# Kernel tuning notes

Measured on AMD Instinct MI355X. Metric: run time of the kernel, lower is better.

Reference implementation:

```python
import jax, jax.numpy as jnp
import numpy as np

N = 4096      # n_nodes
F = 512       # input_dim
R = 64        # repr_dim
H = 8         # n_heads
EPS_BIAS = 0.01
ALPHA = 0.2   # LeakyReLU negative slope
NEG_BIG = 1e16


def setup_inputs() -> dict:
    key = jax.random.key(0)
    k1, k2, k3, k4, k5 = jax.random.split(key, 5)
    node_matrix = jax.random.normal(k1, (N, F), dtype=jnp.float32)
    adjacency_matrix = (jax.random.uniform(k2, (N, N)) < 0.01).astype(jnp.float32)
    adjacency_matrix = jnp.maximum(adjacency_matrix, jnp.eye(N, dtype=jnp.float32))
    # learned parameters (xavier-ish scale)
    W = jax.random.normal(k3, (H, F, R), dtype=jnp.float32) * 0.06
    shared_attention = jax.random.normal(k4, (H, 2 * R), dtype=jnp.float32) * 0.1
    attention_biases = jax.random.normal(k5, (N, N), dtype=jnp.float32) * 0.02
    return {
        "node_matrix": node_matrix,
        "adjacency_matrix": adjacency_matrix,
        "W": W,
        "shared_attention": shared_attention,
        "attention_biases": attention_biases,
    }


def reference(node_matrix, adjacency_matrix, W, shared_attention, attention_biases):
    # hidden_repr: [H, N, R]
    hidden = jnp.einsum('nf,hfr->hnr', node_matrix, W)
    # per-head source/destination scores: [H, N]
    a_src = jnp.einsum('hnr,hr->hn', hidden, shared_attention[:, :R])
    a_dst = jnp.einsum('hnr,hr->hn', hidden, shared_attention[:, R:])
    # broadcast-sum + trainable pair bias: [H, N, N]
    pre = a_src[:, :, None] + a_dst[:, None, :] + EPS_BIAS * attention_biases[None]
    full = jnp.where(pre >= 0, pre, ALPHA * pre)  # LeakyReLU
    # adjacency masking then row softmax
    scores = full + (-NEG_BIG * (1.0 - adjacency_matrix))[None]
    att = jax.nn.softmax(scores, axis=-1)  # [H, N, N]
    # weighted aggregation: [H, N, R]
    out = jnp.einsum('hnm,hmr->hnr', att, hidden)
    # 'concat' aggregation: [N, H*R], head h occupies columns h*R:(h+1)*R
    return jnp.transpose(out, (1, 0, 2)).reshape(N, H * R)
```

## Files before the change

kernel.cpp:

```cpp
#include <hip/hip_runtime.h>
#include <hip/hip_bf16.h>

#define NN 4096
#define FF 512
#define RR 64
#define HH 8
#define HR (HH * RR)
#define CAP 128
#define ATT_STRIDE 144

typedef short bf16x8 __attribute__((ext_vector_type(8)));
typedef float f32x4 __attribute__((ext_vector_type(4)));

__device__ __forceinline__ unsigned short f2bf(float f) {
  __hip_bfloat16 h = __float2bfloat16(f);
  return *reinterpret_cast<unsigned short*>(&h);
}
__device__ __forceinline__ float bf2f(unsigned short u) {
  union { unsigned u32; float f; } cv;
  cv.u32 = ((unsigned)u) << 16;
  return cv.f;
}
__device__ __forceinline__ unsigned nib4(const float4 v) {
  unsigned m = 0;
  if (v.x != 0.f) m |= 1u;
  if (v.y != 0.f) m |= 2u;
  if (v.z != 0.f) m |= 4u;
  if (v.w != 0.f) m |= 8u;
  return m;
}

__global__ __launch_bounds__(256) void k_stream(
    const float* __restrict__ X, const float* __restrict__ W,
    const float* __restrict__ adj,
    unsigned short* __restrict__ Xb, unsigned short* __restrict__ BbT,
    int* __restrict__ colsG, int* __restrict__ cnts)
{
  __shared__ unsigned short wt[64][68];
  const int b = blockIdx.x;
  const int tid = threadIdx.x;

  if (b < 1024) {
    const int lane = tid & 63;
    const int row = b * 4 + (tid >> 6);
    const float* arow = adj + (size_t)row * NN;
    unsigned long long pm = 0;
    {
      float4 buf[8];
#pragma unroll
      for (int c = 0; c < 8; ++c)
        buf[c] = *reinterpret_cast<const float4*>(&arow[c * 256 + (lane << 2)]);
#pragma unroll
      for (int c = 0; c < 8; ++c)
        pm |= (unsigned long long)nib4(buf[c]) << (4 * c);
#pragma unroll
      for (int c = 0; c < 8; ++c)
        buf[c] = *reinterpret_cast<const float4*>(&arow[(c + 8) * 256 + (lane << 2)]);
#pragma unroll
      for (int c = 0; c < 8; ++c)
        pm |= (unsigned long long)nib4(buf[c]) << (4 * c + 32);
    }
    const int cnt = __popcll(pm);
    int pfx = cnt;
#pragma unroll
    for (int off = 1; off < 64; off <<= 1) {
      const int o = __shfl_up(pfx, off);
      if (lane >= off) pfx += o;
    }
    int pos = pfx - cnt;
    unsigned long long m = pm;
    int* cg = colsG + (size_t)row * CAP;
    while (m) {
      const int bit = (int)__builtin_ctzll(m);
      m &= m - 1;
      if (pos < CAP) cg[pos] = ((bit >> 2) << 8) + (lane << 2) + (bit & 3);
      ++pos;
    }
    const int tot = __shfl(pfx, 63);
    for (int p = tot + lane; p < CAP; p += 64) cg[p] = 0;
    if (lane == 63) cnts[row] = tot < CAP ? tot : CAP;
  } else if (b < 3072) {
    const int t = (b - 1024) * 256 + tid;
    const float4 v = reinterpret_cast<const float4*>(X)[t];
    ushort4 u;
    u.x = f2bf(v.x); u.y = f2bf(v.y); u.z = f2bf(v.z); u.w = f2bf(v.w);
    reinterpret_cast<ushort4*>(Xb)[t] = u;
  } else {
    const int b2 = b - 3072;
    const int h = b2 >> 3;
    const int f0 = (b2 & 7) << 6;
    const int fr = tid >> 2;
    const int rq = (tid & 3) << 4;
    const float* wp = W + (size_t)h * FF * RR + (size_t)(f0 + fr) * RR + rq;
#pragma unroll
    for (int v = 0; v < 4; ++v) {
      const float4 x = *reinterpret_cast<const float4*>(wp + v * 4);
      wt[rq + v * 4 + 0][fr] = f2bf(x.x);
      wt[rq + v * 4 + 1][fr] = f2bf(x.y);
      wt[rq + v * 4 + 2][fr] = f2bf(x.z);
      wt[rq + v * 4 + 3][fr] = f2bf(x.w);
    }
    __syncthreads();
    const int r = tid >> 2;
    unsigned short* op = BbT + (size_t)(h * 64 + r) * FF + f0 + ((tid & 3) << 4);
    int4 w0 = *reinterpret_cast<const int4*>(&wt[r][(tid & 3) << 4]);
    int4 w1 = *reinterpret_cast<const int4*>(&wt[r][((tid & 3) << 4) + 8]);
    *reinterpret_cast<int4*>(op) = w0;
    *reinterpret_cast<int4*>(op + 8) = w1;
  }
}

__global__ __launch_bounds__(256) void k_gemm_hidden(
    const unsigned short* __restrict__ Xb,
    const unsigned short* __restrict__ BbT,
    const float* __restrict__ sa,
    unsigned short* __restrict__ hiddenT,
    float* __restrict__ a_srcT,
    float* __restrict__ a_dstT)
{
  const int row0 = blockIdx.x * 64;
  const int h = blockIdx.y;
  const int n0 = h * 64;
  __shared__ unsigned short Als[64 * 32];
  __shared__ unsigned short Bls[64 * 32];
  __shared__ float redS[64][2];
  __shared__ float redD[64][2];
  const int tid = threadIdx.x;
  const int l = tid & 63;
  const int wid = tid >> 6;
  const int wr = wid >> 1, wc = wid & 1;

  f32x4 acc[2][2];
#pragma unroll
  for (int a = 0; a < 2; ++a)
#pragma unroll
    for (int bb = 0; bb < 2; ++bb) acc[a][bb] = (f32x4){0.f, 0.f, 0.f, 0.f};

  const int srow = tid >> 2;
  const int skel = (tid & 3) * 8;

  for (int k0 = 0; k0 < FF; k0 += 32) {
    const int4 av = *reinterpret_cast<const int4*>(
        &Xb[(size_t)(row0 + srow) * FF + k0 + skel]);
    const int4 bv = *reinterpret_cast<const int4*>(
        &BbT[(size_t)(n0 + srow) * FF + k0 + skel]);
    __syncthreads();
    *reinterpret_cast<int4*>(&Als[tid * 8]) = av;
    *reinterpret_cast<int4*>(&Bls[tid * 8]) = bv;
    __syncthreads();

    const int ka = (l >> 4) * 8;
    const bf16x8 a0 = *reinterpret_cast<const bf16x8*>(&Als[(32 * wr + 0  + (l & 15)) * 32 + ka]);
    const bf16x8 a1 = *reinterpret_cast<const bf16x8*>(&Als[(32 * wr + 16 + (l & 15)) * 32 + ka]);
    const bf16x8 b0 = *reinterpret_cast<const bf16x8*>(&Bls[(32 * wc + 0  + (l & 15)) * 32 + ka]);
    const bf16x8 b1 = *reinterpret_cast<const bf16x8*>(&Bls[(32 * wc + 16 + (l & 15)) * 32 + ka]);
    acc[0][0] = __builtin_amdgcn_mfma_f32_16x16x32_bf16(a0, b0, acc[0][0], 0, 0, 0);
    acc[0][1] = __builtin_amdgcn_mfma_f32_16x16x32_bf16(a0, b1, acc[0][1], 0, 0, 0);
    acc[1][0] = __builtin_amdgcn_mfma_f32_16x16x32_bf16(a1, b0, acc[1][0], 0, 0, 0);
    acc[1][1] = __builtin_amdgcn_mfma_f32_16x16x32_bf16(a1, b1, acc[1][1], 0, 0, 0);
  }

  const int lg = l >> 4;
  const int lc = l & 15;

#pragma unroll
  for (int mi = 0; mi < 2; ++mi)
#pragma unroll
    for (int ni = 0; ni < 2; ++ni)
#pragma unroll
      for (int j = 0; j < 4; ++j) {
        const int rowg = row0 + 32 * wr + 16 * mi + (lg << 2) + j;
        const int colg = n0 + 32 * wc + 16 * ni + lc;
        hiddenT[(size_t)rowg * HR + colg] = f2bf(acc[mi][ni][j]);
      }

  float sS[2], sD[2];
#pragma unroll
  for (int ni = 0; ni < 2; ++ni) {
    const int col = 32 * wc + 16 * ni + lc;
    sS[ni] = sa[(size_t)h * 2 * RR + col];
    sD[ni] = sa[(size_t)h * 2 * RR + RR + col];
  }
#pragma unroll
  for (int mi = 0; mi < 2; ++mi)
#pragma unroll
    for (int j = 0; j < 4; ++j) {
      float ps = acc[mi][0][j] * sS[0] + acc[mi][1][j] * sS[1];
      float pd = acc[mi][0][j] * sD[0] + acc[mi][1][j] * sD[1];
#pragma unroll
      for (int off = 8; off >= 1; off >>= 1) {
        ps += __shfl_xor(ps, off);
        pd += __shfl_xor(pd, off);
      }
      if (lc == 0) {
        const int rl = 32 * wr + 16 * mi + (lg << 2) + j;
        redS[rl][wc] = ps;
        redD[rl][wc] = pd;
      }
    }
  __syncthreads();
  if (tid < 64) {
    a_srcT[(size_t)(row0 + tid) * HH + h] = redS[tid][0] + redS[tid][1];
    a_dstT[(size_t)(row0 + tid) * HH + h] = redD[tid][0] + redD[tid][1];
  }
}

__global__ __launch_bounds__(256) void k_gat_row(
    const int* __restrict__ colsG,
    const int* __restrict__ cnts,
    const float* __restrict__ bias,
    const float* __restrict__ a_srcT,
    const float* __restrict__ a_dstT,
    const unsigned short* __restrict__ hiddenT,
    float* __restrict__ out)
{
  const int i = blockIdx.x;
  const int tid = threadIdx.x;

  __shared__ __align__(16) float att[HH][ATT_STRIDE];
  __shared__ int cols[CAP];
  __shared__ __align__(16) float accred[4][HR];

  int c = 0;
  float4 d0, d1;
  float b = 0.f;
  if (tid < CAP) {
    c = colsG[(size_t)i * CAP + tid];
  }
  const int count = cnts[i];
  if (tid < CAP) {
    b = 0.01f * bias[(size_t)i * NN + c];
    d0 = *reinterpret_cast<const float4*>(&a_dstT[(size_t)c * HH]);
    d1 = *reinterpret_cast<const float4*>(&a_dstT[(size_t)c * HH + 4]);
  }
  const float4 s0 = *reinterpret_cast<const float4*>(&a_srcT[(size_t)i * HH]);
  const float4 s1 = *reinterpret_cast<const float4*>(&a_srcT[(size_t)i * HH + 4]);

  if (tid < CAP) {
    cols[tid] = c;
    float s;
    s = s0.x + d0.x + b; att[0][tid] = (s >= 0.f) ? s : 0.2f * s;
    s = s0.y + d0.y + b; att[1][tid] = (s >= 0.f) ? s : 0.2f * s;
    s = s0.z + d0.z + b; att[2][tid] = (s >= 0.f) ? s : 0.2f * s;
    s = s0.w + d0.w + b; att[3][tid] = (s >= 0.f) ? s : 0.2f * s;
    s = s1.x + d1.x + b; att[4][tid] = (s >= 0.f) ? s : 0.2f * s;
    s = s1.y + d1.y + b; att[5][tid] = (s >= 0.f) ? s : 0.2f * s;
    s = s1.z + d1.z + b; att[6][tid] = (s >= 0.f) ? s : 0.2f * s;
    s = s1.w + d1.w + b; att[7][tid] = (s >= 0.f) ? s : 0.2f * s;
  }
  __syncthreads();

  {
    const int g = tid >> 5;
    const int l = tid & 31;
    float* arow_h = att[g];
    float m = -3.0e38f;
    for (int t = l; t < count; t += 32) m = fmaxf(m, arow_h[t]);
#pragma unroll
    for (int o = 16; o >= 1; o >>= 1) m = fmaxf(m, __shfl_xor(m, o));
    float ssum = 0.f;
    for (int t = l; t < count; t += 32) {
      const float e = expf(arow_h[t] - m);
      arow_h[t] = e;
      ssum += e;
    }
#pragma unroll
    for (int o = 16; o >= 1; o >>= 1) ssum += __shfl_xor(ssum, o);
    const float inv = 1.0f / ssum;
    for (int t = l; t < count; t += 32) arow_h[t] *= inv;
  }
  __syncthreads();

  {
    const int g2 = tid >> 6;
    const int o0 = (tid & 63) << 3;
    const float* attrow = att[o0 >> 6];
    const unsigned short* hb = hiddenT + o0;
    const int q = (count + 3) >> 2;
    const int t0 = g2 * q;
    const int t1 = min(t0 + q, count);
    float4 accA = make_float4(0.f, 0.f, 0.f, 0.f);
    float4 accB = make_float4(0.f, 0.f, 0.f, 0.f);
    for (int t = t0; t < t1; ++t) {
      const int cc = cols[t];
      const float a = attrow[t];
      const ushort4 ua = *reinterpret_cast<const ushort4*>(hb + (size_t)cc * HR);
      const ushort4 ub = *reinterpret_cast<const ushort4*>(hb + (size_t)cc * HR + 4);
      accA.x += a * bf2f(ua.x); accA.y += a * bf2f(ua.y);
      accA.z += a * bf2f(ua.z); accA.w += a * bf2f(ua.w);
      accB.x += a * bf2f(ub.x); accB.y += a * bf2f(ub.y);
      accB.z += a * bf2f(ub.z); accB.w += a * bf2f(ub.w);
    }
    *reinterpret_cast<float4*>(&accred[g2][o0]) = accA;
    *reinterpret_cast<float4*>(&accred[g2][o0 + 4]) = accB;
  }
  __syncthreads();
  {
    const int o = tid << 1;
    const float2 r = make_float2(
        accred[0][o] + accred[1][o] + accred[2][o] + accred[3][o],
        accred[0][o + 1] + accred[1][o + 1] + accred[2][o + 1] + accred[3][o + 1]);
    *reinterpret_cast<float2*>(&out[(size_t)i * HR + o]) = r;
  }
}

extern "C" void kernel_launch(void* const* d_in, const int* in_sizes, int n_in,
                              void* d_out, int out_size, void* d_ws, size_t ws_size,
                              hipStream_t stream) {
  const float* X    = (const float*)d_in[0];
  const float* adj  = (const float*)d_in[1];
  const float* W    = (const float*)d_in[2];
  const float* sa   = (const float*)d_in[3];
  const float* bias = (const float*)d_in[4];
  float* out = (float*)d_out;

  unsigned short* hiddenT = (unsigned short*)d_ws;
  unsigned short* Xb  = hiddenT + (size_t)NN * HR;
  unsigned short* BbT = Xb + (size_t)NN * FF;
  float* a_srcT = (float*)(BbT + (size_t)HR * FF);
  float* a_dstT = a_srcT + (size_t)NN * HH;
  int* cnts     = (int*)(a_dstT + (size_t)NN * HH);
  int* colsG    = cnts + NN;

  k_stream<<<dim3(3136), 256, 0, stream>>>(X, W, adj, Xb, BbT, colsG, cnts);
  k_gemm_hidden<<<dim3(NN / 64, HH), 256, 0, stream>>>(Xb, BbT, sa, hiddenT, a_srcT, a_dstT);
  k_gat_row<<<dim3(NN), 256, 0, stream>>>(colsG, cnts, bias, a_srcT, a_dstT, hiddenT, out);
}
```

Baseline: 47.00 us.

## Fuse X bf16 conversion into GEMM and co-schedule with adjacency compaction

Drops the separate pass that writes a bf16 copy of X. The GEMM now reads fp32 X and converts it inline, and it runs in the same launch as the adjacency compaction blocks, with the W transpose split into a small kernel of its own. This removes one round trip of X through memory and lets the GEMM overlap the adjacency streaming. Separately, the aggregation in the row kernel is split 8 ways with 16 columns per thread instead of 4 ways, which raises register use and the size of the reduction in shared memory.

```diff
diff --git a/kernel.cpp b/kernel.cpp
--- a/kernel.cpp
+++ b/kernel.cpp
@@ -30,19 +30,137 @@
   return m;
 }
 
-__global__ __launch_bounds__(256) void k_stream(
-    const float* __restrict__ X, const float* __restrict__ W,
-    const float* __restrict__ adj,
-    unsigned short* __restrict__ Xb, unsigned short* __restrict__ BbT,
+__global__ __launch_bounds__(256) void k_wconv(
+    const float* __restrict__ W, unsigned short* __restrict__ BbT)
+{
+  __shared__ unsigned short wt[64][68];
+  const int b2 = blockIdx.x;
+  const int h = b2 >> 3;
+  const int f0 = (b2 & 7) << 6;
+  const int tid = threadIdx.x;
+  const int fr = tid >> 2;
+  const int rq = (tid & 3) << 4;
+  const float* wp = W + (size_t)h * FF * RR + (size_t)(f0 + fr) * RR + rq;
+#pragma unroll
+  for (int v = 0; v < 4; ++v) {
+    const float4 x = *reinterpret_cast<const float4*>(wp + v * 4);
+    wt[rq + v * 4 + 0][fr] = f2bf(x.x);
+    wt[rq + v * 4 + 1][fr] = f2bf(x.y);
+    wt[rq + v * 4 + 2][fr] = f2bf(x.z);
+    wt[rq + v * 4 + 3][fr] = f2bf(x.w);
+  }
+  __syncthreads();
+  const int r = tid >> 2;
+  unsigned short* op = BbT + (size_t)(h * 64 + r) * FF + f0 + ((tid & 3) << 4);
+  int4 w0 = *reinterpret_cast<const int4*>(&wt[r][(tid & 3) << 4]);
+  int4 w1 = *reinterpret_cast<const int4*>(&wt[r][((tid & 3) << 4) + 8]);
+  *reinterpret_cast<int4*>(op) = w0;
+  *reinterpret_cast<int4*>(op + 8) = w1;
+}
+
+__global__ __launch_bounds__(256) void k_mega(
+    const float* __restrict__ X, const float* __restrict__ adj,
+    const float* __restrict__ sa, const unsigned short* __restrict__ BbT,
+    unsigned short* __restrict__ hiddenT,
+    float* __restrict__ a_srcT, float* __restrict__ a_dstT,
     int* __restrict__ colsG, int* __restrict__ cnts)
 {
-  __shared__ unsigned short wt[64][68];
+  __shared__ unsigned short Als[64 * 32];
+  __shared__ unsigned short Bls[64 * 32];
+  __shared__ float redS[64][2];
+  __shared__ float redD[64][2];
   const int b = blockIdx.x;
   const int tid = threadIdx.x;
 
-  if (b < 1024) {
+  if (b < 512) {
+    const int row0 = (b & 63) * 64;
+    const int h = b >> 6;
+    const int n0 = h * 64;
+    const int l = tid & 63;
+    const int wid = tid >> 6;
+    const int wr = wid >> 1, wc = wid & 1;
+
+    f32x4 acc[2][2];
+#pragma unroll
+    for (int a = 0; a < 2; ++a)
+#pragma unroll
+      for (int bb = 0; bb < 2; ++bb) acc[a][bb] = (f32x4){0.f, 0.f, 0.f, 0.f};
+
+    const int srow = tid >> 2;
+    const int skel = (tid & 3) * 8;
+
+    for (int k0 = 0; k0 < FF; k0 += 32) {
+      const float* xp = &X[(size_t)(row0 + srow) * FF + k0 + skel];
+      const float4 x0 = *reinterpret_cast<const float4*>(xp);
+      const float4 x1 = *reinterpret_cast<const float4*>(xp + 4);
+      const int4 bv = *reinterpret_cast<const int4*>(
+          &BbT[(size_t)(n0 + srow) * FF + k0 + skel]);
+      ushort4 ua, ub;
+      ua.x = f2bf(x0.x); ua.y = f2bf(x0.y); ua.z = f2bf(x0.z); ua.w = f2bf(x0.w);
+      ub.x = f2bf(x1.x); ub.y = f2bf(x1.y); ub.z = f2bf(x1.z); ub.w = f2bf(x1.w);
+      __syncthreads();
+      *reinterpret_cast<ushort4*>(&Als[tid * 8]) = ua;
+      *reinterpret_cast<ushort4*>(&Als[tid * 8 + 4]) = ub;
+      *reinterpret_cast<int4*>(&Bls[tid * 8]) = bv;
+      __syncthreads();
+
+      const int ka = (l >> 4) * 8;
+      const bf16x8 a0 = *reinterpret_cast<const bf16x8*>(&Als[(32 * wr + 0  + (l & 15)) * 32 + ka]);
+      const bf16x8 a1 = *reinterpret_cast<const bf16x8*>(&Als[(32 * wr + 16 + (l & 15)) * 32 + ka]);
+      const bf16x8 b0 = *reinterpret_cast<const bf16x8*>(&Bls[(32 * wc + 0  + (l & 15)) * 32 + ka]);
+      const bf16x8 b1 = *reinterpret_cast<const bf16x8*>(&Bls[(32 * wc + 16 + (l & 15)) * 32 + ka]);
+      acc[0][0] = __builtin_amdgcn_mfma_f32_16x16x32_bf16(a0, b0, acc[0][0], 0, 0, 0);
+      acc[0][1] = __builtin_amdgcn_mfma_f32_16x16x32_bf16(a0, b1, acc[0][1], 0, 0, 0);
+      acc[1][0] = __builtin_amdgcn_mfma_f32_16x16x32_bf16(a1, b0, acc[1][0], 0, 0, 0);
+      acc[1][1] = __builtin_amdgcn_mfma_f32_16x16x32_bf16(a1, b1, acc[1][1], 0, 0, 0);
+    }
+
+    const int lg = l >> 4;
+    const int lc = l & 15;
+
+#pragma unroll
+    for (int mi = 0; mi < 2; ++mi)
+#pragma unroll
+      for (int ni = 0; ni < 2; ++ni)
+#pragma unroll
+        for (int j = 0; j < 4; ++j) {
+          const int rowg = row0 + 32 * wr + 16 * mi + (lg << 2) + j;
+          const int colg = n0 + 32 * wc + 16 * ni + lc;
+          hiddenT[(size_t)rowg * HR + colg] = f2bf(acc[mi][ni][j]);
+        }
+
+    float sS[2], sD[2];
+#pragma unroll
+    for (int ni = 0; ni < 2; ++ni) {
+      const int col = 32 * wc + 16 * ni + lc;
+      sS[ni] = sa[(size_t)h * 2 * RR + col];
+      sD[ni] = sa[(size_t)h * 2 * RR + RR + col];
+    }
+#pragma unroll
+    for (int mi = 0; mi < 2; ++mi)
+#pragma unroll
+      for (int j = 0; j < 4; ++j) {
+        float ps = acc[mi][0][j] * sS[0] + acc[mi][1][j] * sS[1];
+        float pd = acc[mi][0][j] * sD[0] + acc[mi][1][j] * sD[1];
+#pragma unroll
+        for (int off = 8; off >= 1; off >>= 1) {
+          ps += __shfl_xor(ps, off);
+          pd += __shfl_xor(pd, off);
+        }
+        if (lc == 0) {
+          const int rl = 32 * wr + 16 * mi + (lg << 2) + j;
+          redS[rl][wc] = ps;
+          redD[rl][wc] = pd;
+        }
+      }
+    __syncthreads();
+    if (tid < 64) {
+      a_srcT[(size_t)(row0 + tid) * HH + h] = redS[tid][0] + redS[tid][1];
+      a_dstT[(size_t)(row0 + tid) * HH + h] = redD[tid][0] + redD[tid][1];
+    }
+  } else {
     const int lane = tid & 63;
-    const int row = b * 4 + (tid >> 6);
+    const int row = (b - 512) * 4 + (tid >> 6);
     const float* arow = adj + (size_t)row * NN;
     unsigned long long pm = 0;
     {
@@ -79,129 +197,6 @@
     const int tot = __shfl(pfx, 63);
     for (int p = tot + lane; p < CAP; p += 64) cg[p] = 0;
     if (lane == 63) cnts[row] = tot < CAP ? tot : CAP;
-  } else if (b < 3072) {
-    const int t = (b - 1024) * 256 + tid;
-    const float4 v = reinterpret_cast<const float4*>(X)[t];
-    ushort4 u;
-    u.x = f2bf(v.x); u.y = f2bf(v.y); u.z = f2bf(v.z); u.w = f2bf(v.w);
-    reinterpret_cast<ushort4*>(Xb)[t] = u;
-  } else {
-    const int b2 = b - 3072;
-    const int h = b2 >> 3;
-    const int f0 = (b2 & 7) << 6;
-    const int fr = tid >> 2;
-    const int rq = (tid & 3) << 4;
-    const float* wp = W + (size_t)h * FF * RR + (size_t)(f0 + fr) * RR + rq;
-#pragma unroll
-    for (int v = 0; v < 4; ++v) {
-      const float4 x = *reinterpret_cast<const float4*>(wp + v * 4);
-      wt[rq + v * 4 + 0][fr] = f2bf(x.x);
-      wt[rq + v * 4 + 1][fr] = f2bf(x.y);
-      wt[rq + v * 4 + 2][fr] = f2bf(x.z);
-      wt[rq + v * 4 + 3][fr] = f2bf(x.w);
-    }
-    __syncthreads();
-    const int r = tid >> 2;
-    unsigned short* op = BbT + (size_t)(h * 64 + r) * FF + f0 + ((tid & 3) << 4);
-    int4 w0 = *reinterpret_cast<const int4*>(&wt[r][(tid & 3) << 4]);
-    int4 w1 = *reinterpret_cast<const int4*>(&wt[r][((tid & 3) << 4) + 8]);
-    *reinterpret_cast<int4*>(op) = w0;
-    *reinterpret_cast<int4*>(op + 8) = w1;
-  }
-}
-
-__global__ __launch_bounds__(256) void k_gemm_hidden(
-    const unsigned short* __restrict__ Xb,
-    const unsigned short* __restrict__ BbT,
-    const float* __restrict__ sa,
-    unsigned short* __restrict__ hiddenT,
-    float* __restrict__ a_srcT,
-    float* __restrict__ a_dstT)
-{
-  const int row0 = blockIdx.x * 64;
-  const int h = blockIdx.y;
-  const int n0 = h * 64;
-  __shared__ unsigned short Als[64 * 32];
-  __shared__ unsigned short Bls[64 * 32];
-  __shared__ float redS[64][2];
-  __shared__ float redD[64][2];
-  const int tid = threadIdx.x;
-  const int l = tid & 63;
-  const int wid = tid >> 6;
-  const int wr = wid >> 1, wc = wid & 1;
-
-  f32x4 acc[2][2];
-#pragma unroll
-  for (int a = 0; a < 2; ++a)
-#pragma unroll
-    for (int bb = 0; bb < 2; ++bb) acc[a][bb] = (f32x4){0.f, 0.f, 0.f, 0.f};
-
-  const int srow = tid >> 2;
-  const int skel = (tid & 3) * 8;
-
-  for (int k0 = 0; k0 < FF; k0 += 32) {
-    const int4 av = *reinterpret_cast<const int4*>(
-        &Xb[(size_t)(row0 + srow) * FF + k0 + skel]);
-    const int4 bv = *reinterpret_cast<const int4*>(
-        &BbT[(size_t)(n0 + srow) * FF + k0 + skel]);
-    __syncthreads();
-    *reinterpret_cast<int4*>(&Als[tid * 8]) = av;
-    *reinterpret_cast<int4*>(&Bls[tid * 8]) = bv;
-    __syncthreads();
-
-    const int ka = (l >> 4) * 8;
-    const bf16x8 a0 = *reinterpret_cast<const bf16x8*>(&Als[(32 * wr + 0  + (l & 15)) * 32 + ka]);
-    const bf16x8 a1 = *reinterpret_cast<const bf16x8*>(&Als[(32 * wr + 16 + (l & 15)) * 32 + ka]);
-    const bf16x8 b0 = *reinterpret_cast<const bf16x8*>(&Bls[(32 * wc + 0  + (l & 15)) * 32 + ka]);
-    const bf16x8 b1 = *reinterpret_cast<const bf16x8*>(&Bls[(32 * wc + 16 + (l & 15)) * 32 + ka]);
-    acc[0][0] = __builtin_amdgcn_mfma_f32_16x16x32_bf16(a0, b0, acc[0][0], 0, 0, 0);
-    acc[0][1] = __builtin_amdgcn_mfma_f32_16x16x32_bf16(a0, b1, acc[0][1], 0, 0, 0);
-    acc[1][0] = __builtin_amdgcn_mfma_f32_16x16x32_bf16(a1, b0, acc[1][0], 0, 0, 0);
-    acc[1][1] = __builtin_amdgcn_mfma_f32_16x16x32_bf16(a1, b1, acc[1][1], 0, 0, 0);
-  }
-
-  const int lg = l >> 4;
-  const int lc = l & 15;
-
-#pragma unroll
-  for (int mi = 0; mi < 2; ++mi)
-#pragma unroll
-    for (int ni = 0; ni < 2; ++ni)
-#pragma unroll
-      for (int j = 0; j < 4; ++j) {
-        const int rowg = row0 + 32 * wr + 16 * mi + (lg << 2) + j;
-        const int colg = n0 + 32 * wc + 16 * ni + lc;
-        hiddenT[(size_t)rowg * HR + colg] = f2bf(acc[mi][ni][j]);
-      }
-
-  float sS[2], sD[2];
-#pragma unroll
-  for (int ni = 0; ni < 2; ++ni) {
-    const int col = 32 * wc + 16 * ni + lc;
-    sS[ni] = sa[(size_t)h * 2 * RR + col];
-    sD[ni] = sa[(size_t)h * 2 * RR + RR + col];
-  }
-#pragma unroll
-  for (int mi = 0; mi < 2; ++mi)
-#pragma unroll
-    for (int j = 0; j < 4; ++j) {
-      float ps = acc[mi][0][j] * sS[0] + acc[mi][1][j] * sS[1];
-      float pd = acc[mi][0][j] * sD[0] + acc[mi][1][j] * sD[1];
-#pragma unroll
-      for (int off = 8; off >= 1; off >>= 1) {
-        ps += __shfl_xor(ps, off);
-        pd += __shfl_xor(pd, off);
-      }
-      if (lc == 0) {
-        const int rl = 32 * wr + 16 * mi + (lg << 2) + j;
-        redS[rl][wc] = ps;
-        redD[rl][wc] = pd;
-      }
-    }
-  __syncthreads();
-  if (tid < 64) {
-    a_srcT[(size_t)(row0 + tid) * HH + h] = redS[tid][0] + redS[tid][1];
-    a_dstT[(size_t)(row0 + tid) * HH + h] = redD[tid][0] + redD[tid][1];
   }
 }
 
@@ -219,14 +214,12 @@
 
   __shared__ __align__(16) float att[HH][ATT_STRIDE];
   __shared__ int cols[CAP];
-  __shared__ __align__(16) float accred[4][HR];
+  __shared__ __align__(16) float accred[8][HR];
 
   int c = 0;
   float4 d0, d1;
   float b = 0.f;
-  if (tid < CAP) {
-    c = colsG[(size_t)i * CAP + tid];
-  }
+  if (tid < CAP) c = colsG[(size_t)i * CAP + tid];
   const int count = cnts[i];
   if (tid < CAP) {
     b = 0.01f * bias[(size_t)i * NN + c];
@@ -272,35 +265,49 @@
   __syncthreads();
 
   {
-    const int g2 = tid >> 6;
-    const int o0 = (tid & 63) << 3;
+    const int g2 = tid >> 5;
+    const int o0 = (tid & 31) << 4;
     const float* attrow = att[o0 >> 6];
     const unsigned short* hb = hiddenT + o0;
-    const int q = (count + 3) >> 2;
+    const int q = (count + 7) >> 3;
     const int t0 = g2 * q;
     const int t1 = min(t0 + q, count);
-    float4 accA = make_float4(0.f, 0.f, 0.f, 0.f);
-    float4 accB = make_float4(0.f, 0.f, 0.f, 0.f);
+    float acc[16];
+#pragma unroll
+    for (int j = 0; j < 16; ++j) acc[j] = 0.f;
     for (int t = t0; t < t1; ++t) {
       const int cc = cols[t];
       const float a = attrow[t];
-      const ushort4 ua = *reinterpret_cast<const ushort4*>(hb + (size_t)cc * HR);
-      const ushort4 ub = *reinterpret_cast<const ushort4*>(hb + (size_t)cc * HR + 4);
-      accA.x += a * bf2f(ua.x); accA.y += a * bf2f(ua.y);
-      accA.z += a * bf2f(ua.z); accA.w += a * bf2f(ua.w);
-      accB.x += a * bf2f(ub.x); accB.y += a * bf2f(ub.y);
-      accB.z += a * bf2f(ub.z); accB.w += a * bf2f(ub.w);
-    }
-    *reinterpret_cast<float4*>(&accred[g2][o0]) = accA;
-    *reinterpret_cast<float4*>(&accred[g2][o0 + 4]) = accB;
+      const unsigned short* hp = hb + (size_t)cc * HR;
+      const ushort4 u0 = *reinterpret_cast<const ushort4*>(hp);
+      const ushort4 u1 = *reinterpret_cast<const ushort4*>(hp + 4);
+      const ushort4 u2 = *reinterpret_cast<const ushort4*>(hp + 8);
+      const ushort4 u3 = *reinterpret_cast<const ushort4*>(hp + 12);
+      acc[0] += a * bf2f(u0.x);  acc[1] += a * bf2f(u0.y);
+      acc[2] += a * bf2f(u0.z);  acc[3] += a * bf2f(u0.w);
+      acc[4] += a * bf2f(u1.x);  acc[5] += a * bf2f(u1.y);
+      acc[6] += a * bf2f(u1.z);  acc[7] += a * bf2f(u1.w);
+      acc[8] += a * bf2f(u2.x);  acc[9] += a * bf2f(u2.y);
+      acc[10] += a * bf2f(u2.z); acc[11] += a * bf2f(u2.w);
+      acc[12] += a * bf2f(u3.x); acc[13] += a * bf2f(u3.y);
+      acc[14] += a * bf2f(u3.z); acc[15] += a * bf2f(u3.w);
+    }
+#pragma unroll
+    for (int j = 0; j < 4; ++j) {
+      float4 v = make_float4(acc[j * 4], acc[j * 4 + 1], acc[j * 4 + 2], acc[j * 4 + 3]);
+      *reinterpret_cast<float4*>(&accred[g2][o0 + j * 4]) = v;
+    }
   }
   __syncthreads();
   {
     const int o = tid << 1;
-    const float2 r = make_float2(
-        accred[0][o] + accred[1][o] + accred[2][o] + accred[3][o],
-        accred[0][o + 1] + accred[1][o + 1] + accred[2][o + 1] + accred[3][o + 1]);
-    *reinterpret_cast<float2*>(&out[(size_t)i * HR + o]) = r;
+    float r0 = 0.f, r1 = 0.f;
+#pragma unroll
+    for (int g = 0; g < 8; ++g) {
+      const float2 v = *reinterpret_cast<const float2*>(&accred[g][o]);
+      r0 += v.x; r1 += v.y;
+    }
+    *reinterpret_cast<float2*>(&out[(size_t)i * HR + o]) = make_float2(r0, r1);
   }
 }
 
@@ -315,14 +322,13 @@
   float* out = (float*)d_out;
 
   unsigned short* hiddenT = (unsigned short*)d_ws;
-  unsigned short* Xb  = hiddenT + (size_t)NN * HR;
-  unsigned short* BbT = Xb + (size_t)NN * FF;
+  unsigned short* BbT = hiddenT + (size_t)NN * HR;
   float* a_srcT = (float*)(BbT + (size_t)HR * FF);
   float* a_dstT = a_srcT + (size_t)NN * HH;
   int* cnts     = (int*)(a_dstT + (size_t)NN * HH);
   int* colsG    = cnts + NN;
 
-  k_stream<<<dim3(3136), 256, 0, stream>>>(X, W, adj, Xb, BbT, colsG, cnts);
-  k_gemm_hidden<<<dim3(NN / 64, HH), 256, 0, stream>>>(Xb, BbT, sa, hiddenT, a_srcT, a_dstT);
+  k_wconv<<<dim3(64), 256, 0, stream>>>(W, BbT);
+  k_mega<<<dim3(1536), 256, 0, stream>>>(X, adj, sa, BbT, hiddenT, a_srcT, a_dstT, colsG, cnts);
   k_gat_row<<<dim3(NN), 256, 0, stream>>>(colsG, cnts, bias, a_srcT, a_dstT, hiddenT, out);
 }
```

Measured after the change: 48.35 us. 1.03x slower.

## Overlap adjacency compaction with hidden GEMM by merging them into one kernel

Applied to the files above, without the earlier changes.

The adjacency scan that builds the per-row column lists moves out of the convert kernel and into the GEMM kernel as extra blocks. The first 512 blocks do the GEMM and the remaining 1024 blocks compact the adjacency rows. The memory-bound 64 MB adjacency read can then run concurrently with the compute-bound GEMM, and the convert kernel becomes small. The trade-off is that the merged kernel carries the GEMM's shared-memory footprint for the scan blocks, and scheduling order depends on block dispatch.

```diff
diff --git a/kernel.cpp b/kernel.cpp
--- a/kernel.cpp
+++ b/kernel.cpp
@@ -30,19 +30,147 @@
   return m;
 }
 
-__global__ __launch_bounds__(256) void k_stream(
+__global__ __launch_bounds__(256) void k_convert(
     const float* __restrict__ X, const float* __restrict__ W,
-    const float* __restrict__ adj,
-    unsigned short* __restrict__ Xb, unsigned short* __restrict__ BbT,
-    int* __restrict__ colsG, int* __restrict__ cnts)
+    unsigned short* __restrict__ Xb, unsigned short* __restrict__ BbT)
 {
   __shared__ unsigned short wt[64][68];
   const int b = blockIdx.x;
   const int tid = threadIdx.x;
 
-  if (b < 1024) {
+  if (b < 2048) {
+    const int t = b * 256 + tid;
+    const float4 v = reinterpret_cast<const float4*>(X)[t];
+    ushort4 u;
+    u.x = f2bf(v.x); u.y = f2bf(v.y); u.z = f2bf(v.z); u.w = f2bf(v.w);
+    reinterpret_cast<ushort4*>(Xb)[t] = u;
+  } else {
+    const int b2 = b - 2048;
+    const int h = b2 >> 3;
+    const int f0 = (b2 & 7) << 6;
+    const int fr = tid >> 2;
+    const int rq = (tid & 3) << 4;
+    const float* wp = W + (size_t)h * FF * RR + (size_t)(f0 + fr) * RR + rq;
+#pragma unroll
+    for (int v = 0; v < 4; ++v) {
+      const float4 x = *reinterpret_cast<const float4*>(wp + v * 4);
+      wt[rq + v * 4 + 0][fr] = f2bf(x.x);
+      wt[rq + v * 4 + 1][fr] = f2bf(x.y);
+      wt[rq + v * 4 + 2][fr] = f2bf(x.z);
+      wt[rq + v * 4 + 3][fr] = f2bf(x.w);
+    }
+    __syncthreads();
+    const int r = tid >> 2;
+    unsigned short* op = BbT + (size_t)(h * 64 + r) * FF + f0 + ((tid & 3) << 4);
+    int4 w0 = *reinterpret_cast<const int4*>(&wt[r][(tid & 3) << 4]);
+    int4 w1 = *reinterpret_cast<const int4*>(&wt[r][((tid & 3) << 4) + 8]);
+    *reinterpret_cast<int4*>(op) = w0;
+    *reinterpret_cast<int4*>(op + 8) = w1;
+  }
+}
+
+__global__ __launch_bounds__(256) void k_mega(
+    const unsigned short* __restrict__ Xb,
+    const unsigned short* __restrict__ BbT,
+    const float* __restrict__ sa,
+    const float* __restrict__ adj,
+    unsigned short* __restrict__ hiddenT,
+    float* __restrict__ a_srcT,
+    float* __restrict__ a_dstT,
+    int* __restrict__ colsG,
+    int* __restrict__ cnts)
+{
+  __shared__ unsigned short Als[64 * 32];
+  __shared__ unsigned short Bls[64 * 32];
+  __shared__ float redS[64][2];
+  __shared__ float redD[64][2];
+  const int b = blockIdx.x;
+  const int tid = threadIdx.x;
+
+  if (b < 512) {
+    const int row0 = (b & 63) * 64;
+    const int h = b >> 6;
+    const int n0 = h * 64;
+    const int l = tid & 63;
+    const int wid = tid >> 6;
+    const int wr = wid >> 1, wc = wid & 1;
+
+    f32x4 acc[2][2];
+#pragma unroll
+    for (int a = 0; a < 2; ++a)
+#pragma unroll
+      for (int bb = 0; bb < 2; ++bb) acc[a][bb] = (f32x4){0.f, 0.f, 0.f, 0.f};
+
+    const int srow = tid >> 2;
+    const int skel = (tid & 3) * 8;
+
+    for (int k0 = 0; k0 < FF; k0 += 32) {
+      const int4 av = *reinterpret_cast<const int4*>(
+          &Xb[(size_t)(row0 + srow) * FF + k0 + skel]);
+      const int4 bv = *reinterpret_cast<const int4*>(
+          &BbT[(size_t)(n0 + srow) * FF + k0 + skel]);
+      __syncthreads();
+      *reinterpret_cast<int4*>(&Als[tid * 8]) = av;
+      *reinterpret_cast<int4*>(&Bls[tid * 8]) = bv;
+      __syncthreads();
+
+      const int ka = (l >> 4) * 8;
+      const bf16x8 a0 = *reinterpret_cast<const bf16x8*>(&Als[(32 * wr + 0  + (l & 15)) * 32 + ka]);
+      const bf16x8 a1 = *reinterpret_cast<const bf16x8*>(&Als[(32 * wr + 16 + (l & 15)) * 32 + ka]);
+      const bf16x8 b0 = *reinterpret_cast<const bf16x8*>(&Bls[(32 * wc + 0  + (l & 15)) * 32 + ka]);
+      const bf16x8 b1 = *reinterpret_cast<const bf16x8*>(&Bls[(32 * wc + 16 + (l & 15)) * 32 + ka]);
+      acc[0][0] = __builtin_amdgcn_mfma_f32_16x16x32_bf16(a0, b0, acc[0][0], 0, 0, 0);
+      acc[0][1] = __builtin_amdgcn_mfma_f32_16x16x32_bf16(a0, b1, acc[0][1], 0, 0, 0);
+      acc[1][0] = __builtin_amdgcn_mfma_f32_16x16x32_bf16(a1, b0, acc[1][0], 0, 0, 0);
+      acc[1][1] = __builtin_amdgcn_mfma_f32_16x16x32_bf16(a1, b1, acc[1][1], 0, 0, 0);
+    }
+
+    const int lg = l >> 4;
+    const int lc = l & 15;
+
+#pragma unroll
+    for (int mi = 0; mi < 2; ++mi)
+#pragma unroll
+      for (int ni = 0; ni < 2; ++ni)
+#pragma unroll
+        for (int j = 0; j < 4; ++j) {
+          const int rowg = row0 + 32 * wr + 16 * mi + (lg << 2) + j;
+          const int colg = n0 + 32 * wc + 16 * ni + lc;
+          hiddenT[(size_t)rowg * HR + colg] = f2bf(acc[mi][ni][j]);
+        }
+
+    float sS[2], sD[2];
+#pragma unroll
+    for (int ni = 0; ni < 2; ++ni) {
+      const int col = 32 * wc + 16 * ni + lc;
+      sS[ni] = sa[(size_t)h * 2 * RR + col];
+      sD[ni] = sa[(size_t)h * 2 * RR + RR + col];
+    }
+#pragma unroll
+    for (int mi = 0; mi < 2; ++mi)
+#pragma unroll
+      for (int j = 0; j < 4; ++j) {
+        float ps = acc[mi][0][j] * sS[0] + acc[mi][1][j] * sS[1];
+        float pd = acc[mi][0][j] * sD[0] + acc[mi][1][j] * sD[1];
+#pragma unroll
+        for (int off = 8; off >= 1; off >>= 1) {
+          ps += __shfl_xor(ps, off);
+          pd += __shfl_xor(pd, off);
+        }
+        if (lc == 0) {
+          const int rl = 32 * wr + 16 * mi + (lg << 2) + j;
+          redS[rl][wc] = ps;
+          redD[rl][wc] = pd;
+        }
+      }
+    __syncthreads();
+    if (tid < 64) {
+      a_srcT[(size_t)(row0 + tid) * HH + h] = redS[tid][0] + redS[tid][1];
+      a_dstT[(size_t)(row0 + tid) * HH + h] = redD[tid][0] + redD[tid][1];
+    }
+  } else {
     const int lane = tid & 63;
-    const int row = b * 4 + (tid >> 6);
+    const int row = (b - 512) * 4 + (tid >> 6);
     const float* arow = adj + (size_t)row * NN;
     unsigned long long pm = 0;
     {
@@ -79,129 +207,6 @@
     const int tot = __shfl(pfx, 63);
     for (int p = tot + lane; p < CAP; p += 64) cg[p] = 0;
     if (lane == 63) cnts[row] = tot < CAP ? tot : CAP;
-  } else if (b < 3072) {
-    const int t = (b - 1024) * 256 + tid;
-    const float4 v = reinterpret_cast<const float4*>(X)[t];
-    ushort4 u;
-    u.x = f2bf(v.x); u.y = f2bf(v.y); u.z = f2bf(v.z); u.w = f2bf(v.w);
-    reinterpret_cast<ushort4*>(Xb)[t] = u;
-  } else {
-    const int b2 = b - 3072;
-    const int h = b2 >> 3;
-    const int f0 = (b2 & 7) << 6;
-    const int fr = tid >> 2;
-    const int rq = (tid & 3) << 4;
-    const float* wp = W + (size_t)h * FF * RR + (size_t)(f0 + fr) * RR + rq;
-#pragma unroll
-    for (int v = 0; v < 4; ++v) {
-      const float4 x = *reinterpret_cast<const float4*>(wp + v * 4);
-      wt[rq + v * 4 + 0][fr] = f2bf(x.x);
-      wt[rq + v * 4 + 1][fr] = f2bf(x.y);
-      wt[rq + v * 4 + 2][fr] = f2bf(x.z);
-      wt[rq + v * 4 + 3][fr] = f2bf(x.w);
-    }
-    __syncthreads();
-    const int r = tid >> 2;
-    unsigned short* op = BbT + (size_t)(h * 64 + r) * FF + f0 + ((tid & 3) << 4);
-    int4 w0 = *reinterpret_cast<const int4*>(&wt[r][(tid & 3) << 4]);
-    int4 w1 = *reinterpret_cast<const int4*>(&wt[r][((tid & 3) << 4) + 8]);
-    *reinterpret_cast<int4*>(op) = w0;
-    *reinterpret_cast<int4*>(op + 8) = w1;
-  }
-}
-
-__global__ __launch_bounds__(256) void k_gemm_hidden(
-    const unsigned short* __restrict__ Xb,
-    const unsigned short* __restrict__ BbT,
-    const float* __restrict__ sa,
-    unsigned short* __restrict__ hiddenT,
-    float* __restrict__ a_srcT,
-    float* __restrict__ a_dstT)
-{
-  const int row0 = blockIdx.x * 64;
-  const int h = blockIdx.y;
-  const int n0 = h * 64;
-  __shared__ unsigned short Als[64 * 32];
-  __shared__ unsigned short Bls[64 * 32];
-  __shared__ float redS[64][2];
-  __shared__ float redD[64][2];
-  const int tid = threadIdx.x;
-  const int l = tid & 63;
-  const int wid = tid >> 6;
-  const int wr = wid >> 1, wc = wid & 1;
-
-  f32x4 acc[2][2];
-#pragma unroll
-  for (int a = 0; a < 2; ++a)
-#pragma unroll
-    for (int bb = 0; bb < 2; ++bb) acc[a][bb] = (f32x4){0.f, 0.f, 0.f, 0.f};
-
-  const int srow = tid >> 2;
-  const int skel = (tid & 3) * 8;
-
-  for (int k0 = 0; k0 < FF; k0 += 32) {
-    const int4 av = *reinterpret_cast<const int4*>(
-        &Xb[(size_t)(row0 + srow) * FF + k0 + skel]);
-    const int4 bv = *reinterpret_cast<const int4*>(
-        &BbT[(size_t)(n0 + srow) * FF + k0 + skel]);
-    __syncthreads();
-    *reinterpret_cast<int4*>(&Als[tid * 8]) = av;
-    *reinterpret_cast<int4*>(&Bls[tid * 8]) = bv;
-    __syncthreads();
-
-    const int ka = (l >> 4) * 8;
-    const bf16x8 a0 = *reinterpret_cast<const bf16x8*>(&Als[(32 * wr + 0  + (l & 15)) * 32 + ka]);
-    const bf16x8 a1 = *reinterpret_cast<const bf16x8*>(&Als[(32 * wr + 16 + (l & 15)) * 32 + ka]);
-    const bf16x8 b0 = *reinterpret_cast<const bf16x8*>(&Bls[(32 * wc + 0  + (l & 15)) * 32 + ka]);
-    const bf16x8 b1 = *reinterpret_cast<const bf16x8*>(&Bls[(32 * wc + 16 + (l & 15)) * 32 + ka]);
-    acc[0][0] = __builtin_amdgcn_mfma_f32_16x16x32_bf16(a0, b0, acc[0][0], 0, 0, 0);
-    acc[0][1] = __builtin_amdgcn_mfma_f32_16x16x32_bf16(a0, b1, acc[0][1], 0, 0, 0);
-    acc[1][0] = __builtin_amdgcn_mfma_f32_16x16x32_bf16(a1, b0, acc[1][0], 0, 0, 0);
-    acc[1][1] = __builtin_amdgcn_mfma_f32_16x16x32_bf16(a1, b1, acc[1][1], 0, 0, 0);
-  }
-
-  const int lg = l >> 4;
-  const int lc = l & 15;
-
-#pragma unroll
-  for (int mi = 0; mi < 2; ++mi)
-#pragma unroll
-    for (int ni = 0; ni < 2; ++ni)
-#pragma unroll
-      for (int j = 0; j < 4; ++j) {
-        const int rowg = row0 + 32 * wr + 16 * mi + (lg << 2) + j;
-        const int colg = n0 + 32 * wc + 16 * ni + lc;
-        hiddenT[(size_t)rowg * HR + colg] = f2bf(acc[mi][ni][j]);
-      }
-
-  float sS[2], sD[2];
-#pragma unroll
-  for (int ni = 0; ni < 2; ++ni) {
-    const int col = 32 * wc + 16 * ni + lc;
-    sS[ni] = sa[(size_t)h * 2 * RR + col];
-    sD[ni] = sa[(size_t)h * 2 * RR + RR + col];
-  }
-#pragma unroll
-  for (int mi = 0; mi < 2; ++mi)
-#pragma unroll
-    for (int j = 0; j < 4; ++j) {
-      float ps = acc[mi][0][j] * sS[0] + acc[mi][1][j] * sS[1];
-      float pd = acc[mi][0][j] * sD[0] + acc[mi][1][j] * sD[1];
-#pragma unroll
-      for (int off = 8; off >= 1; off >>= 1) {
-        ps += __shfl_xor(ps, off);
-        pd += __shfl_xor(pd, off);
-      }
-      if (lc == 0) {
-        const int rl = 32 * wr + 16 * mi + (lg << 2) + j;
-        redS[rl][wc] = ps;
-        redD[rl][wc] = pd;
-      }
-    }
-  __syncthreads();
-  if (tid < 64) {
-    a_srcT[(size_t)(row0 + tid) * HH + h] = redS[tid][0] + redS[tid][1];
-    a_dstT[(size_t)(row0 + tid) * HH + h] = redD[tid][0] + redD[tid][1];
   }
 }
 
@@ -224,9 +229,7 @@
   int c = 0;
   float4 d0, d1;
   float b = 0.f;
-  if (tid < CAP) {
-    c = colsG[(size_t)i * CAP + tid];
-  }
+  if (tid < CAP) c = colsG[(size_t)i * CAP + tid];
   const int count = cnts[i];
   if (tid < CAP) {
     b = 0.01f * bias[(size_t)i * NN + c];
@@ -322,7 +325,7 @@
   int* cnts     = (int*)(a_dstT + (size_t)NN * HH);
   int* colsG    = cnts + NN;
 
-  k_stream<<<dim3(3136), 256, 0, stream>>>(X, W, adj, Xb, BbT, colsG, cnts);
-  k_gemm_hidden<<<dim3(NN / 64, HH), 256, 0, stream>>>(Xb, BbT, sa, hiddenT, a_srcT, a_dstT);
+  k_convert<<<dim3(2112), 256, 0, stream>>>(X, W, Xb, BbT);
+  k_mega<<<dim3(1536), 256, 0, stream>>>(Xb, BbT, sa, adj, hiddenT, a_srcT, a_dstT, colsG, cnts);
   k_gat_row<<<dim3(NN), 256, 0, stream>>>(colsG, cnts, bias, a_srcT, a_dstT, hiddenT, out);
 }
```

Measured after the change: 46.11 us. About the same (-1.9%).
